# Performance work log

Hardware: AMD Instinct MI355X
Metric: run time of the kernel (lower is better)

Reference implementation:

```python
import jax, jax.numpy as jnp
import numpy as np

# Static 4-level feature pyramid (H, W) per level; total tokens = 20197
SHAPES = [(100, 152), (50, 76), (25, 38), (13, 19)]
B, S, E, H, L, P, R = 4, 1024, 256, 8, 4, 20, 4
HD = E // H
OFFSET_SCALE = 4.0


def setup_inputs() -> dict:
    key = jax.random.key(0)
    ks = jax.random.split(key, 11)
    total = sum(h * w for h, w in SHAPES)
    s = 0.02
    return {
        "x": jax.random.normal(ks[0], (B, S, E), jnp.float32),
        "encoder_input": jax.random.normal(ks[1], (B, total, E), jnp.float32),
        "v_w": jax.random.normal(ks[2], (E, E), jnp.float32) * s,
        "out_w": jax.random.normal(ks[3], (E, E), jnp.float32) * s,
        "off_w": jax.random.normal(ks[4], (H * L * P * 2, E), jnp.float32) * s,
        "off_b": jax.random.normal(ks[5], (H * L * P * 2,), jnp.float32) * s,
        "attn_w": jax.random.normal(ks[6], (H * L * P, E), jnp.float32) * s,
        "attn_b": jax.random.normal(ks[7], (H * L * P,), jnp.float32) * s,
        "ref_w": jax.random.normal(ks[8], (H * R, E), jnp.float32) * s,
        "ref_b": jax.random.normal(ks[9], (H * R,), jnp.float32) * s,
        "def_refs": jax.random.uniform(ks[10], (R, 2), jnp.float32, 0.1, 0.9),
        "spatial_shapes": jnp.array(SHAPES, dtype=jnp.int32),
    }


def _grid_sample(img, gx, gy, Hh, Ww):
    """Bilinear grid_sample, padding_mode='zeros', align_corners=False.
    img: (N, C, Hh*Ww); gx, gy: (N, M) in [-1, 1]. Returns (N, C, M)."""
    x = ((gx + 1.0) * Ww - 1.0) * 0.5
    y = ((gy + 1.0) * Hh - 1.0) * 0.5
    x0 = jnp.floor(x)
    y0 = jnp.floor(y)
    wx = x - x0
    wy = y - y0
    x0i = x0.astype(jnp.int32)
    y0i = y0.astype(jnp.int32)
    N, C, _ = img.shape

    def gather(xi, yi):
        valid = (xi >= 0) & (xi < Ww) & (yi >= 0) & (yi < Hh)
        idx = jnp.clip(yi, 0, Hh - 1) * Ww + jnp.clip(xi, 0, Ww - 1)
        v = jnp.take_along_axis(
            img, jnp.broadcast_to(idx[:, None, :], (N, C, idx.shape[-1])), axis=2)
        return v * valid[:, None, :].astype(img.dtype)

    return (gather(x0i, y0i) * ((1 - wx) * (1 - wy))[:, None, :]
            + gather(x0i + 1, y0i) * (wx * (1 - wy))[:, None, :]
            + gather(x0i, y0i + 1) * ((1 - wx) * wy)[:, None, :]
            + gather(x0i + 1, y0i + 1) * (wx * wy)[:, None, :])


def reference(x, encoder_input, v_w, out_w, off_w, off_b, attn_w, attn_b,
              ref_w, ref_b, def_refs, spatial_shapes):
    b, s, _ = x.shape
    values = (encoder_input @ v_w.T).reshape(b, -1, H, HD)
    refs = jax.nn.sigmoid(def_refs)  # (R, 2), default reference points
    ref_mix = jax.nn.softmax((x @ ref_w.T + ref_b).reshape(b, s, H, R), axis=-1)
    anchors = jnp.einsum('bshr,rc->bshc', ref_mix, refs)  # (b, s, H, 2)
    offsets = (x @ off_w.T + off_b).reshape(b, s, H, L, P, 2)
    attn = jax.nn.softmax((x @ attn_w.T + attn_b).reshape(b, s, H, L * P),
                          axis=-1).reshape(b, s, H, L, P)

    out = jnp.zeros((b, s, H, HD), x.dtype)
    start = 0
    for lvl, (hh, ww) in enumerate(SHAPES):  # static per-level loop (L=4)
        img = values[:, start:start + hh * ww]  # (b, hh*ww, H, HD)
        start += hh * ww
        img = img.transpose(0, 2, 3, 1).reshape(b * H, HD, hh * ww)
        norm = jnp.array([max(ww, 1), max(hh, 1)], x.dtype)
        locs = anchors[:, :, :, None, :] + jnp.tanh(offsets[:, :, :, lvl]) * (OFFSET_SCALE / norm)
        grid = jnp.clip(locs, 0.0, 1.0) * 2.0 - 1.0  # (b, s, H, P, 2)
        grid = grid.transpose(0, 2, 1, 3, 4).reshape(b * H, s * P, 2)
        sampled = _grid_sample(img, grid[..., 0], grid[..., 1], hh, ww)  # (b*H, HD, s*P)
        sampled = sampled.reshape(b, H, HD, s, P)
        out = out + jnp.einsum('bhcsp,bshp->bshc', sampled, attn[:, :, :, lvl])
    return out.reshape(b, s, E) @ out_w.T
```

## Files before the change

kernel.cpp:

```cpp
#include <hip/hip_runtime.h>
#include <hip/hip_bf16.h>
#include <math.h>

#define NH 8
#define HD 32
#define EDIM 256
#define NL 4
#define NP 20
#define NR 4
#define SEQ 1024
#define BATCH 4
#define TOTAL 20197
#define OFF_SCALE 4.0f

#define M_ENC (BATCH * TOTAL)
#define KDIM 256
#define LDSW 40

typedef short bf16x8 __attribute__((ext_vector_type(8)));
typedef float f32x4  __attribute__((ext_vector_type(4)));

__device__ __forceinline__ unsigned short f32_to_bf16_rne(float f) {
    unsigned u = __float_as_uint(f);
    return (unsigned short)((u + 0x7fffu + ((u >> 16) & 1u)) >> 16);
}

__global__ __launch_bounds__(256) void cast3_kernel(
    const float* __restrict__ s0, unsigned short* __restrict__ d0, long n0,
    const float* __restrict__ s1, unsigned short* __restrict__ d1, long n1,
    const float* __restrict__ s2, unsigned short* __restrict__ d2, long n2)
{
    long c0 = n0 >> 3, c1 = n1 >> 3, c2 = n2 >> 3;
    long total = c0 + c1 + c2;
    long gid = (long)blockIdx.x * blockDim.x + threadIdx.x;
    long stride = (long)gridDim.x * blockDim.x;
    for (long i = gid; i < total; i += stride) {
        const float* s; unsigned short* d; long e;
        if (i < c0)            { s = s0; d = d0; e = i * 8; }
        else if (i < c0 + c1)  { s = s1; d = d1; e = (i - c0) * 8; }
        else                   { s = s2; d = d2; e = (i - c0 - c1) * 8; }
        float4 a = *reinterpret_cast<const float4*>(s + e);
        float4 b = *reinterpret_cast<const float4*>(s + e + 4);
        float f[8] = {a.x, a.y, a.z, a.w, b.x, b.y, b.z, b.w};
        unsigned short o[8];
        #pragma unroll
        for (int j = 0; j < 8; ++j) o[j] = f32_to_bf16_rne(f[j]);
        *reinterpret_cast<uint4*>(d + e) = *reinterpret_cast<const uint4*>(o);
    }
}

__global__ __launch_bounds__(256) void gemm_mfma_f32a_kernel(
    const float* __restrict__ A,
    const unsigned short* __restrict__ W,
    const float* __restrict__ bias,
    float* __restrict__ C,
    int M_real, int N)
{
    __shared__ __align__(16) unsigned short As[2][128 * LDSW];
    __shared__ __align__(16) unsigned short Ws[2][128 * LDSW];

    const int tid  = threadIdx.x;
    const int m0   = blockIdx.x * 128;
    const int n0   = blockIdx.y * 128;
    const int wave = tid >> 6;
    const int lane = tid & 63;
    const int wr   = wave >> 1;
    const int wc   = wave & 1;
    const int lrow = lane & 15;
    const int kg   = lane >> 4;

    const int arow = tid >> 3;
    const int asl  = tid & 7;
    const int wrow = tid >> 2;
    const int wks  = tid & 3;

    f32x4  acc[4][4] = {};
    float4 areg[4];
    uint4  wreg[2];

    auto LOADT = [&](int t) {
        const int k0 = t * 32;
        #pragma unroll
        for (int p = 0; p < 4; ++p) {
            int gm = m0 + arow + 32 * p;
            float4 v = make_float4(0.f, 0.f, 0.f, 0.f);
            if (gm < M_real)
                v = *reinterpret_cast<const float4*>(
                    &A[(size_t)gm * KDIM + k0 + asl * 4]);
            areg[p] = v;
        }
        #pragma unroll
        for (int it = 0; it < 2; ++it)
            wreg[it] = *reinterpret_cast<const uint4*>(
                &W[(size_t)(n0 + wrow + 64 * it) * KDIM + k0 + wks * 8]);
    };
    auto STORE = [&](int b) {
        #pragma unroll
        for (int p = 0; p < 4; ++p) {
            unsigned short o[4] = {
                f32_to_bf16_rne(areg[p].x), f32_to_bf16_rne(areg[p].y),
                f32_to_bf16_rne(areg[p].z), f32_to_bf16_rne(areg[p].w)};
            *reinterpret_cast<uint2*>(&As[b][(arow + 32 * p) * LDSW + asl * 4]) =
                *reinterpret_cast<const uint2*>(o);
        }
        #pragma unroll
        for (int it = 0; it < 2; ++it)
            *reinterpret_cast<uint4*>(&Ws[b][(wrow + 64 * it) * LDSW + wks * 8]) =
                wreg[it];
    };
    auto COMPUTE = [&](int b) {
        bf16x8 af[4], bfr[4];
        #pragma unroll
        for (int mi = 0; mi < 4; ++mi)
            af[mi] = *reinterpret_cast<const bf16x8*>(
                &As[b][(wr * 64 + mi * 16 + lrow) * LDSW + kg * 8]);
        #pragma unroll
        for (int nj = 0; nj < 4; ++nj)
            bfr[nj] = *reinterpret_cast<const bf16x8*>(
                &Ws[b][(wc * 64 + nj * 16 + lrow) * LDSW + kg * 8]);
        #pragma unroll
        for (int mi = 0; mi < 4; ++mi)
            #pragma unroll
            for (int nj = 0; nj < 4; ++nj)
                acc[mi][nj] = __builtin_amdgcn_mfma_f32_16x16x32_bf16(
                    af[mi], bfr[nj], acc[mi][nj], 0, 0, 0);
    };

    LOADT(0);
    STORE(0);
    __syncthreads();
    #pragma unroll
    for (int t = 0; t < 8; ++t) {
        if (t < 7) LOADT(t + 1);
        COMPUTE(t & 1);
        if (t < 7) {
            STORE((t + 1) & 1);
            __syncthreads();
        }
    }

    #pragma unroll
    for (int mi = 0; mi < 4; ++mi) {
        #pragma unroll
        for (int nj = 0; nj < 4; ++nj) {
            int row_base = m0 + wr * 64 + mi * 16 + kg * 4;
            int col      = n0 + wc * 64 + nj * 16 + lrow;
            float bv = bias ? bias[col] : 0.f;
            #pragma unroll
            for (int r = 0; r < 4; ++r) {
                int row = row_base + r;
                if (row < M_real)
                    C[(size_t)row * N + col] = acc[mi][nj][r] + bv;
            }
        }
    }
}

__global__ __launch_bounds__(256) void gemm_atb_kernel(
    const float* __restrict__ A, const float* __restrict__ W,
    const float* __restrict__ bias, float* __restrict__ C,
    int M, int N, int K)
{
    __shared__ float As[16][64];
    __shared__ float Wt[16][64];

    const int tid = threadIdx.x;
    const int m0 = blockIdx.x * 64;
    const int n0 = blockIdx.y * 64;
    const int tx = tid & 15;
    const int ty = tid >> 4;
    const int lr = tid >> 2;
    const int lk = (tid & 3) << 2;

    const int am = m0 + lr;
    const int wn = n0 + lr;

    float acc[4][4] = {};

    for (int k0 = 0; k0 < K; k0 += 16) {
        float4 av = make_float4(0.f, 0.f, 0.f, 0.f);
        float4 wv = make_float4(0.f, 0.f, 0.f, 0.f);
        if (am < M) av = *reinterpret_cast<const float4*>(&A[(size_t)am * K + k0 + lk]);
        if (wn < N) wv = *reinterpret_cast<const float4*>(&W[(size_t)wn * K + k0 + lk]);
        As[lk + 0][lr] = av.x; As[lk + 1][lr] = av.y;
        As[lk + 2][lr] = av.z; As[lk + 3][lr] = av.w;
        Wt[lk + 0][lr] = wv.x; Wt[lk + 1][lr] = wv.y;
        Wt[lk + 2][lr] = wv.z; Wt[lk + 3][lr] = wv.w;
        __syncthreads();

        #pragma unroll
        for (int k = 0; k < 16; ++k) {
            float a[4], b[4];
            #pragma unroll
            for (int i = 0; i < 4; ++i) a[i] = As[k][ty * 4 + i];
            #pragma unroll
            for (int j = 0; j < 4; ++j) b[j] = Wt[k][tx * 4 + j];
            #pragma unroll
            for (int i = 0; i < 4; ++i)
                #pragma unroll
                for (int j = 0; j < 4; ++j)
                    acc[i][j] += a[i] * b[j];
        }
        __syncthreads();
    }

    #pragma unroll
    for (int i = 0; i < 4; ++i) {
        int m = m0 + ty * 4 + i;
        if (m >= M) continue;
        #pragma unroll
        for (int j = 0; j < 4; ++j) {
            int n = n0 + tx * 4 + j;
            if (n >= N) continue;
            float v = acc[i][j];
            if (bias) v += bias[n];
            C[(size_t)m * N + n] = v;
        }
    }
}

__global__ __launch_bounds__(256) void deform_sample_kernel(
    const float* __restrict__ values,
    const float* __restrict__ x,
    const float* __restrict__ ref_w,
    const float* __restrict__ ref_b,
    const float* __restrict__ proj_off,
    const float* __restrict__ proj_attn,
    const float* __restrict__ def_refs,
    float* __restrict__ out)
{
    const int row = blockIdx.x;
    const int b   = row >> 10;
    const int tid = threadIdx.x;

    __shared__ float  attn_s[NH * NL * NP];
    __shared__ float  anchors[NH][2];
    __shared__ float  refv[NH * NR];
    __shared__ __align__(16) unsigned int sidx[NH * NL * NP][4];
    __shared__ float4 wcor[NH * NL * NP];

    if (tid >= 96) {
        int i = tid - 96;
        reinterpret_cast<float4*>(attn_s)[i] =
            reinterpret_cast<const float4*>(proj_attn + (size_t)row * 640)[i];
    } else if (tid < 32) {
        float dot = ref_b[tid];
        const float* xr = x + (size_t)row * 256;
        const float* wr = ref_w + (size_t)tid * 256;
        for (int k = 0; k < 256; k += 4) {
            float4 xv = *reinterpret_cast<const float4*>(xr + k);
            float4 wv = *reinterpret_cast<const float4*>(wr + k);
            dot += xv.x * wv.x; dot += xv.y * wv.y;
            dot += xv.z * wv.z; dot += xv.w * wv.w;
        }
        refv[tid] = dot;
    }
    __syncthreads();

    if (tid < NH) {
        const int h = tid;
        float rv[NR];
        float rmax = -1e30f;
        #pragma unroll
        for (int r = 0; r < NR; ++r) {
            rv[r] = refv[h * NR + r];
            rmax = fmaxf(rmax, rv[r]);
        }
        float rsum = 0.f;
        #pragma unroll
        for (int r = 0; r < NR; ++r) { rv[r] = __expf(rv[r] - rmax); rsum += rv[r]; }
        float ax = 0.f, ay = 0.f;
        #pragma unroll
        for (int r = 0; r < NR; ++r) {
            float pr = rv[r] / rsum;
            float sx = 1.f / (1.f + __expf(-def_refs[r * 2 + 0]));
            float sy = 1.f / (1.f + __expf(-def_refs[r * 2 + 1]));
            ax += pr * sx; ay += pr * sy;
        }
        anchors[h][0] = ax; anchors[h][1] = ay;
    }
    {
        const int g = tid >> 5;
        const int l = tid & 31;
        float v0 = attn_s[g * 80 + l];
        float v1 = attn_s[g * 80 + 32 + l];
        float v2 = (l < 16) ? attn_s[g * 80 + 64 + l] : -1e30f;
        float m = fmaxf(fmaxf(v0, v1), v2);
        #pragma unroll
        for (int d = 16; d >= 1; d >>= 1) m = fmaxf(m, __shfl_xor(m, d, 64));
        float e0 = __expf(v0 - m), e1 = __expf(v1 - m);
        float e2 = (l < 16) ? __expf(v2 - m) : 0.f;
        float s = e0 + e1 + e2;
        #pragma unroll
        for (int d = 16; d >= 1; d >>= 1) s += __shfl_xor(s, d, 64);
        float inv = 1.f / s;
        __syncthreads();
        attn_s[g * 80 + l]      = e0 * inv;
        attn_s[g * 80 + 32 + l] = e1 * inv;
        if (l < 16) attn_s[g * 80 + 64 + l] = e2 * inv;
    }
    __syncthreads();

    const int lhh[NL] = {100, 50, 25, 13};
    const int lww[NL] = {152, 76, 38, 19};
    const int lst[NL] = {0, 15200, 19000, 19950};

    for (int e = tid; e < NH * NL * NP; e += 256) {
        int h = e / 80;
        int rem = e - h * 80;
        int l = rem / 20;
        const float2 o = *reinterpret_cast<const float2*>(
            proj_off + (size_t)row * 1280 + e * 2);
        float offx = tanhf(o.x);
        float offy = tanhf(o.y);
        int ww = lww[l], hh = lhh[l];
        float locx = fminf(fmaxf(anchors[h][0] + offx * (OFF_SCALE / (float)ww), 0.f), 1.f);
        float locy = fminf(fmaxf(anchors[h][1] + offy * (OFF_SCALE / (float)hh), 0.f), 1.f);
        float xx = locx * (float)ww - 0.5f;
        float yy = locy * (float)hh - 0.5f;
        float x0f = floorf(xx), y0f = floorf(yy);
        int x0 = (int)x0f, y0 = (int)y0f;
        float wx = xx - x0f, wy = yy - y0f;
        float wa = attn_s[e];

        float bx0 = (x0 >= 0)      ? 1.f : 0.f;
        float bx1 = (x0 < ww - 1)  ? 1.f : 0.f;
        float by0 = (y0 >= 0)      ? 1.f : 0.f;
        float by1 = (y0 < hh - 1)  ? 1.f : 0.f;
        int xc0 = max(x0, 0), xc1 = min(x0 + 1, ww - 1);
        int yc0 = max(y0, 0), yc1 = min(y0 + 1, hh - 1);
        sidx[e][0] = (unsigned int)(lst[l] + yc0 * ww + xc0) << 8;
        sidx[e][1] = (unsigned int)(lst[l] + yc0 * ww + xc1) << 8;
        sidx[e][2] = (unsigned int)(lst[l] + yc1 * ww + xc0) << 8;
        sidx[e][3] = (unsigned int)(lst[l] + yc1 * ww + xc1) << 8;

        float4 w;
        w.x = wa * (1.f - wx) * (1.f - wy) * bx0 * by0;
        w.y = wa * wx * (1.f - wy) * bx1 * by0;
        w.z = wa * (1.f - wx) * wy * bx0 * by1;
        w.w = wa * wx * wy * bx1 * by1;
        wcor[e] = w;
    }
    __syncthreads();

    const int h = tid >> 5;
    const int c = tid & 31;
    const float* vb = values + (size_t)b * TOTAL * 256 + h * 32 + c;
    float acc = 0.f;
    #pragma unroll 4
    for (int i = 0; i < 80; ++i) {
        int e = h * 80 + i;
        uint4 pi = *reinterpret_cast<const uint4*>(&sidx[e][0]);
        float4 w = wcor[e];
        acc += w.x * vb[pi.x];
        acc += w.y * vb[pi.y];
        acc += w.z * vb[pi.z];
        acc += w.w * vb[pi.w];
    }
    out[(size_t)row * 256 + h * 32 + c] = acc;
}

extern "C" void kernel_launch(void* const* d_in, const int* in_sizes, int n_in,
                              void* d_out, int out_size, void* d_ws, size_t ws_size,
                              hipStream_t stream)
{
    const float* x        = (const float*)d_in[0];
    const float* enc      = (const float*)d_in[1];
    const float* v_w      = (const float*)d_in[2];
    const float* out_w    = (const float*)d_in[3];
    const float* off_w    = (const float*)d_in[4];
    const float* off_b    = (const float*)d_in[5];
    const float* attn_w   = (const float*)d_in[6];
    const float* attn_b   = (const float*)d_in[7];
    const float* ref_w    = (const float*)d_in[8];
    const float* ref_b    = (const float*)d_in[9];
    const float* def_refs = (const float*)d_in[10];
    float* out = (float*)d_out;

    const int M_Q    = BATCH * SEQ;
    const int N_OFF  = NH * NL * NP * 2;
    const int N_ATTN = NH * NL * NP;

    float* ws = (float*)d_ws;
    float* values    = ws;
    float* proj_off  = values    + (size_t)M_ENC * EDIM;
    float* proj_attn = proj_off  + (size_t)M_Q * N_OFF;
    float* attn_out  = proj_attn + (size_t)M_Q * N_ATTN;
    unsigned short* vw_bf16    = (unsigned short*)(attn_out + (size_t)M_Q * EDIM);
    unsigned short* offw_bf16  = vw_bf16   + (size_t)EDIM * KDIM;
    unsigned short* attnw_bf16 = offw_bf16 + (size_t)N_OFF * KDIM;

    dim3 blk(256);

    cast3_kernel<<<dim3(272), blk, 0, stream>>>(
        v_w, vw_bf16, (long)EDIM * KDIM,
        off_w, offw_bf16, (long)N_OFF * KDIM,
        attn_w, attnw_bf16, (long)N_ATTN * KDIM);

    gemm_mfma_f32a_kernel<<<dim3((M_ENC + 127) / 128, EDIM / 128), blk, 0, stream>>>(
        enc, vw_bf16, nullptr, values, M_ENC, EDIM);

    gemm_mfma_f32a_kernel<<<dim3(M_Q / 128, N_OFF / 128), blk, 0, stream>>>(
        x, offw_bf16, off_b, proj_off, M_Q, N_OFF);
    gemm_mfma_f32a_kernel<<<dim3(M_Q / 128, N_ATTN / 128), blk, 0, stream>>>(
        x, attnw_bf16, attn_b, proj_attn, M_Q, N_ATTN);

    deform_sample_kernel<<<dim3(M_Q), blk, 0, stream>>>(
        values, x, ref_w, ref_b, proj_off, proj_attn, def_refs, attn_out);

    gemm_atb_kernel<<<dim3(M_Q / 64, EDIM / 64), blk, 0, stream>>>(
        attn_out, out_w, nullptr, out, M_Q, EDIM, EDIM);
}
```

Measured before the change: 329.6 us.

## Pre-cast encoder input to bf16, run output projection on MFMA, reuse workspace

The encoder input is converted to bf16 by a separate cast pass, and the value-projection GEMM then reads bf16 A directly. The kernel it uses is single-buffered, with no register prefetch. The deform sampling kernel now writes its output in bf16, and the final output projection moves from the scalar fp32 tiled GEMM to the bf16 MFMA kernel with an out_w cast. The query-side GEMMs also lose double buffering, and workspace regions are aliased so enc_bf16 shares space with proj_off and proj_attn. This trades an extra full pass over the encoder tensor, plus lost load/compute overlap, for halved A traffic in the largest GEMM and tensor-core use in the final GEMM.

Result: no change. 329.3 us (-0.1%).

```diff
diff --git a/kernel.cpp b/kernel.cpp
--- a/kernel.cpp
+++ b/kernel.cpp
@@ -49,15 +49,15 @@
     }
 }
 
-__global__ __launch_bounds__(256) void gemm_mfma_f32a_kernel(
-    const float* __restrict__ A,
+__global__ __launch_bounds__(256) void gemm_bf16a_kernel(
+    const unsigned short* __restrict__ A,
     const unsigned short* __restrict__ W,
     const float* __restrict__ bias,
     float* __restrict__ C,
     int M_real, int N)
 {
-    __shared__ __align__(16) unsigned short As[2][128 * LDSW];
-    __shared__ __align__(16) unsigned short Ws[2][128 * LDSW];
+    __shared__ __align__(16) unsigned short As[128 * LDSW];
+    __shared__ __align__(16) unsigned short Ws[128 * LDSW];
 
     const int tid  = threadIdx.x;
     const int m0   = blockIdx.x * 128;
@@ -69,74 +69,42 @@
     const int lrow = lane & 15;
     const int kg   = lane >> 4;
 
-    const int arow = tid >> 3;
-    const int asl  = tid & 7;
-    const int wrow = tid >> 2;
-    const int wks  = tid & 3;
-
-    f32x4  acc[4][4] = {};
-    float4 areg[4];
-    uint4  wreg[2];
-
-    auto LOADT = [&](int t) {
-        const int k0 = t * 32;
-        #pragma unroll
-        for (int p = 0; p < 4; ++p) {
-            int gm = m0 + arow + 32 * p;
-            float4 v = make_float4(0.f, 0.f, 0.f, 0.f);
+    f32x4 acc[4][4] = {};
+
+    for (int k0 = 0; k0 < KDIM; k0 += 32) {
+        #pragma unroll
+        for (int it = 0; it < 2; ++it) {
+            int s   = tid + it * 256;
+            int row = s >> 2;
+            int ks  = s & 3;
+            int gm  = m0 + row;
+            uint4 va = make_uint4(0u, 0u, 0u, 0u);
             if (gm < M_real)
-                v = *reinterpret_cast<const float4*>(
-                    &A[(size_t)gm * KDIM + k0 + asl * 4]);
-            areg[p] = v;
-        }
-        #pragma unroll
-        for (int it = 0; it < 2; ++it)
-            wreg[it] = *reinterpret_cast<const uint4*>(
-                &W[(size_t)(n0 + wrow + 64 * it) * KDIM + k0 + wks * 8]);
-    };
-    auto STORE = [&](int b) {
-        #pragma unroll
-        for (int p = 0; p < 4; ++p) {
-            unsigned short o[4] = {
-                f32_to_bf16_rne(areg[p].x), f32_to_bf16_rne(areg[p].y),
-                f32_to_bf16_rne(areg[p].z), f32_to_bf16_rne(areg[p].w)};
-            *reinterpret_cast<uint2*>(&As[b][(arow + 32 * p) * LDSW + asl * 4]) =
-                *reinterpret_cast<const uint2*>(o);
-        }
-        #pragma unroll
-        for (int it = 0; it < 2; ++it)
-            *reinterpret_cast<uint4*>(&Ws[b][(wrow + 64 * it) * LDSW + wks * 8]) =
-                wreg[it];
-    };
-    auto COMPUTE = [&](int b) {
+                va = *reinterpret_cast<const uint4*>(
+                    A + (size_t)gm * KDIM + k0 + ks * 8);
+            uint4 vw = *reinterpret_cast<const uint4*>(
+                W + (size_t)(n0 + row) * KDIM + k0 + ks * 8);
+            *reinterpret_cast<uint4*>(&As[row * LDSW + ks * 8]) = va;
+            *reinterpret_cast<uint4*>(&Ws[row * LDSW + ks * 8]) = vw;
+        }
+        __syncthreads();
+
         bf16x8 af[4], bfr[4];
         #pragma unroll
         for (int mi = 0; mi < 4; ++mi)
             af[mi] = *reinterpret_cast<const bf16x8*>(
-                &As[b][(wr * 64 + mi * 16 + lrow) * LDSW + kg * 8]);
+                &As[(wr * 64 + mi * 16 + lrow) * LDSW + kg * 8]);
         #pragma unroll
         for (int nj = 0; nj < 4; ++nj)
             bfr[nj] = *reinterpret_cast<const bf16x8*>(
-                &Ws[b][(wc * 64 + nj * 16 + lrow) * LDSW + kg * 8]);
+                &Ws[(wc * 64 + nj * 16 + lrow) * LDSW + kg * 8]);
         #pragma unroll
         for (int mi = 0; mi < 4; ++mi)
             #pragma unroll
             for (int nj = 0; nj < 4; ++nj)
                 acc[mi][nj] = __builtin_amdgcn_mfma_f32_16x16x32_bf16(
                     af[mi], bfr[nj], acc[mi][nj], 0, 0, 0);
-    };
-
-    LOADT(0);
-    STORE(0);
-    __syncthreads();
-    #pragma unroll
-    for (int t = 0; t < 8; ++t) {
-        if (t < 7) LOADT(t + 1);
-        COMPUTE(t & 1);
-        if (t < 7) {
-            STORE((t + 1) & 1);
-            __syncthreads();
-        }
+        __syncthreads();
     }
 
     #pragma unroll
@@ -156,65 +124,86 @@
     }
 }
 
-__global__ __launch_bounds__(256) void gemm_atb_kernel(
-    const float* __restrict__ A, const float* __restrict__ W,
-    const float* __restrict__ bias, float* __restrict__ C,
-    int M, int N, int K)
+__global__ __launch_bounds__(256) void gemm_mfma_f32a_kernel(
+    const float* __restrict__ A,
+    const unsigned short* __restrict__ W,
+    const float* __restrict__ bias,
+    float* __restrict__ C,
+    int M_real, int N)
 {
-    __shared__ float As[16][64];
-    __shared__ float Wt[16][64];
-
-    const int tid = threadIdx.x;
-    const int m0 = blockIdx.x * 64;
-    const int n0 = blockIdx.y * 64;
-    const int tx = tid & 15;
-    const int ty = tid >> 4;
-    const int lr = tid >> 2;
-    const int lk = (tid & 3) << 2;
-
-    const int am = m0 + lr;
-    const int wn = n0 + lr;
-
-    float acc[4][4] = {};
-
-    for (int k0 = 0; k0 < K; k0 += 16) {
-        float4 av = make_float4(0.f, 0.f, 0.f, 0.f);
-        float4 wv = make_float4(0.f, 0.f, 0.f, 0.f);
-        if (am < M) av = *reinterpret_cast<const float4*>(&A[(size_t)am * K + k0 + lk]);
-        if (wn < N) wv = *reinterpret_cast<const float4*>(&W[(size_t)wn * K + k0 + lk]);
-        As[lk + 0][lr] = av.x; As[lk + 1][lr] = av.y;
-        As[lk + 2][lr] = av.z; As[lk + 3][lr] = av.w;
-        Wt[lk + 0][lr] = wv.x; Wt[lk + 1][lr] = wv.y;
-        Wt[lk + 2][lr] = wv.z; Wt[lk + 3][lr] = wv.w;
+    __shared__ __align__(16) unsigned short As[128 * LDSW];
+    __shared__ __align__(16) unsigned short Ws[128 * LDSW];
+
+    const int tid  = threadIdx.x;
+    const int m0   = blockIdx.x * 128;
+    const int n0   = blockIdx.y * 128;
+    const int wave = tid >> 6;
+    const int lane = tid & 63;
+    const int wr   = wave >> 1;
+    const int wc   = wave & 1;
+    const int lrow = lane & 15;
+    const int kg   = lane >> 4;
+
+    f32x4 acc[4][4] = {};
+
+    for (int k0 = 0; k0 < KDIM; k0 += 32) {
+        #pragma unroll
+        for (int p = 0; p < 4; ++p) {
+            int s   = tid + p * 256;
+            int row = s >> 3;
+            int sl  = s & 7;
+            int gm  = m0 + row;
+            float4 v = make_float4(0.f, 0.f, 0.f, 0.f);
+            if (gm < M_real)
+                v = *reinterpret_cast<const float4*>(&A[(size_t)gm * KDIM + k0 + sl * 4]);
+            unsigned short o[4] = {
+                f32_to_bf16_rne(v.x), f32_to_bf16_rne(v.y),
+                f32_to_bf16_rne(v.z), f32_to_bf16_rne(v.w)};
+            *reinterpret_cast<uint2*>(&As[row * LDSW + sl * 4]) =
+                *reinterpret_cast<const uint2*>(o);
+        }
+        #pragma unroll
+        for (int it = 0; it < 2; ++it) {
+            int s   = tid + it * 256;
+            int row = s >> 2;
+            int ks  = s & 3;
+            uint4 vw = *reinterpret_cast<const uint4*>(
+                W + (size_t)(n0 + row) * KDIM + k0 + ks * 8);
+            *reinterpret_cast<uint4*>(&Ws[row * LDSW + ks * 8]) = vw;
+        }
         __syncthreads();
 
-        #pragma unroll
-        for (int k = 0; k < 16; ++k) {
-            float a[4], b[4];
+        bf16x8 af[4], bfr[4];
+        #pragma unroll
+        for (int mi = 0; mi < 4; ++mi)
+            af[mi] = *reinterpret_cast<const bf16x8*>(
+                &As[(wr * 64 + mi * 16 + lrow) * LDSW + kg * 8]);
+        #pragma unroll
+        for (int nj = 0; nj < 4; ++nj)
+            bfr[nj] = *reinterpret_cast<const bf16x8*>(
+                &Ws[(wc * 64 + nj * 16 + lrow) * LDSW + kg * 8]);
+        #pragma unroll
+        for (int mi = 0; mi < 4; ++mi)
             #pragma unroll
-            for (int i = 0; i < 4; ++i) a[i] = As[k][ty * 4 + i];
+            for (int nj = 0; nj < 4; ++nj)
+                acc[mi][nj] = __builtin_amdgcn_mfma_f32_16x16x32_bf16(
+                    af[mi], bfr[nj], acc[mi][nj], 0, 0, 0);
+        __syncthreads();
+    }
+
+    #pragma unroll
+    for (int mi = 0; mi < 4; ++mi) {
+        #pragma unroll
+        for (int nj = 0; nj < 4; ++nj) {
+            int row_base = m0 + wr * 64 + mi * 16 + kg * 4;
+            int col      = n0 + wc * 64 + nj * 16 + lrow;
+            float bv = bias ? bias[col] : 0.f;
             #pragma unroll
-            for (int j = 0; j < 4; ++j) b[j] = Wt[k][tx * 4 + j];
-            #pragma unroll
-            for (int i = 0; i < 4; ++i)
-                #pragma unroll
-                for (int j = 0; j < 4; ++j)
-                    acc[i][j] += a[i] * b[j];
-        }
-        __syncthreads();
-    }
-
-    #pragma unroll
-    for (int i = 0; i < 4; ++i) {
-        int m = m0 + ty * 4 + i;
-        if (m >= M) continue;
-        #pragma unroll
-        for (int j = 0; j < 4; ++j) {
-            int n = n0 + tx * 4 + j;
-            if (n >= N) continue;
-            float v = acc[i][j];
-            if (bias) v += bias[n];
-            C[(size_t)m * N + n] = v;
+            for (int r = 0; r < 4; ++r) {
+                int row = row_base + r;
+                if (row < M_real)
+                    C[(size_t)row * N + col] = acc[mi][nj][r] + bv;
+            }
         }
     }
 }
@@ -227,7 +216,7 @@
     const float* __restrict__ proj_off,
     const float* __restrict__ proj_attn,
     const float* __restrict__ def_refs,
-    float* __restrict__ out)
+    unsigned short* __restrict__ out)
 {
     const int row = blockIdx.x;
     const int b   = row >> 10;
@@ -357,7 +346,7 @@
         acc += w.z * vb[pi.z];
         acc += w.w * vb[pi.w];
     }
-    out[(size_t)row * 256 + h * 32 + c] = acc;
+    out[(size_t)row * 256 + h * 32 + c] = f32_to_bf16_rne(acc);
 }
 
 extern "C" void kernel_launch(void* const* d_in, const int* in_sizes, int n_in,
@@ -382,23 +371,31 @@
     const int N_ATTN = NH * NL * NP;
 
     float* ws = (float*)d_ws;
-    float* values    = ws;
-    float* proj_off  = values    + (size_t)M_ENC * EDIM;
+    float* values = ws;
+    char*  region = (char*)(values + (size_t)M_ENC * EDIM);
+    unsigned short* enc_bf16 = (unsigned short*)region;
+    float* proj_off  = (float*)region;
     float* proj_attn = proj_off  + (size_t)M_Q * N_OFF;
-    float* attn_out  = proj_attn + (size_t)M_Q * N_ATTN;
-    unsigned short* vw_bf16    = (unsigned short*)(attn_out + (size_t)M_Q * EDIM);
-    unsigned short* offw_bf16  = vw_bf16   + (size_t)EDIM * KDIM;
-    unsigned short* attnw_bf16 = offw_bf16 + (size_t)N_OFF * KDIM;
+    unsigned short* attn_out_bf16 = (unsigned short*)(proj_attn + (size_t)M_Q * N_ATTN);
+    unsigned short* offw_bf16  = attn_out_bf16 + (size_t)M_Q * EDIM;
+    unsigned short* attnw_bf16 = offw_bf16  + (size_t)N_OFF * KDIM;
+    unsigned short* outw_bf16  = attnw_bf16 + (size_t)N_ATTN * KDIM;
+    unsigned short* vw_bf16 = (unsigned short*)(region + (size_t)M_ENC * KDIM * 2);
 
     dim3 blk(256);
 
-    cast3_kernel<<<dim3(272), blk, 0, stream>>>(
+    cast3_kernel<<<dim3(2048), blk, 0, stream>>>(
+        enc, enc_bf16, (long)M_ENC * KDIM,
         v_w, vw_bf16, (long)EDIM * KDIM,
+        v_w, vw_bf16, 0L);
+
+    gemm_bf16a_kernel<<<dim3((M_ENC + 127) / 128, EDIM / 128), blk, 0, stream>>>(
+        enc_bf16, vw_bf16, nullptr, values, M_ENC, EDIM);
+
+    cast3_kernel<<<dim3(288), blk, 0, stream>>>(
         off_w, offw_bf16, (long)N_OFF * KDIM,
-        attn_w, attnw_bf16, (long)N_ATTN * KDIM);
-
-    gemm_mfma_f32a_kernel<<<dim3((M_ENC + 127) / 128, EDIM / 128), blk, 0, stream>>>(
-        enc, vw_bf16, nullptr, values, M_ENC, EDIM);
+        attn_w, attnw_bf16, (long)N_ATTN * KDIM,
+        out_w, outw_bf16, (long)EDIM * KDIM);
 
     gemm_mfma_f32a_kernel<<<dim3(M_Q / 128, N_OFF / 128), blk, 0, stream>>>(
         x, offw_bf16, off_b, proj_off, M_Q, N_OFF);
@@ -406,8 +403,8 @@
         x, attnw_bf16, attn_b, proj_attn, M_Q, N_ATTN);
 
     deform_sample_kernel<<<dim3(M_Q), blk, 0, stream>>>(
-        values, x, ref_w, ref_b, proj_off, proj_attn, def_refs, attn_out);
-
-    gemm_atb_kernel<<<dim3(M_Q / 64, EDIM / 64), blk, 0, stream>>>(
-        attn_out, out_w, nullptr, out, M_Q, EDIM, EDIM);
-}
+        values, x, ref_w, ref_b, proj_off, proj_attn, def_refs, attn_out_bf16);
+
+    gemm_bf16a_kernel<<<dim3(M_Q / 128, EDIM / 128), blk, 0, stream>>>(
+        attn_out_bf16, outw_bf16, nullptr, out, M_Q, EDIM);
+}
```
